# Optimization experiments

Measured on AMD Instinct MI355X. Metric: run time of the kernel, lower is better.

## Reference

```python
import jax, jax.numpy as jnp
import numpy as np

N = 50000      # nodes
E = 1600000    # edges (avg degree 32)
F_IN = 3       # PROTEINS num_node_features
H = 64         # dim_h
G = 512        # num graphs in batch
C = 2          # PROTEINS num_classes
BN_EPS = 1e-5


def setup_inputs() -> dict:
    key = jax.random.key(0)
    ks = iter(jax.random.split(key, 64))

    def rn(shape, s=0.1):
        return (jax.random.normal(next(ks), shape) * s).astype(jnp.float32)

    inp = {"x": rn((N, F_IN), 1.0)}
    for li, din in ((1, F_IN), (2, H), (3, H)):
        p = f"conv{li}_"
        inp[p + "w1"] = rn((din, H))
        inp[p + "b1"] = rn((H,))
        inp[p + "bn_g"] = jnp.ones((H,), jnp.float32)
        inp[p + "bn_b"] = jnp.zeros((H,), jnp.float32)
        inp[p + "bn_m"] = rn((H,))
        inp[p + "bn_v"] = jax.random.uniform(next(ks), (H,), jnp.float32, 0.5, 1.5)
        inp[p + "w2"] = rn((H, H))
        inp[p + "b2"] = rn((H,))
    inp["lin1_w"] = rn((3 * H, 3 * H))
    inp["lin1_b"] = rn((3 * H,))
    inp["lin2_w"] = rn((3 * H, C))
    inp["lin2_b"] = rn((C,))
    inp["edge_index"] = jax.random.randint(next(ks), (2, E), 0, N, jnp.int64)
    inp["batch"] = jnp.sort(jax.random.randint(next(ks), (N,), 0, G, jnp.int64))
    return inp


def gin_conv(x, src, dst, w1, b1, g, bb, m, v, w2, b2):
    # GINConv, eps=0: mlp(x + sum_{j->i} x_j); aggregate messages at target (dst)
    agg = jax.ops.segment_sum(x[src], dst, num_segments=N)  # [N, d]
    h = x + agg
    h = h @ w1 + b1
    h = (h - m) * jax.lax.rsqrt(v + BN_EPS) * g + bb  # BatchNorm1d (eval)
    h = jax.nn.relu(h)
    h = jax.nn.relu(h @ w2 + b2)
    return h


def reference(x,
              conv1_w1, conv1_b1, conv1_bn_g, conv1_bn_b, conv1_bn_m, conv1_bn_v, conv1_w2, conv1_b2,
              conv2_w1, conv2_b1, conv2_bn_g, conv2_bn_b, conv2_bn_m, conv2_bn_v, conv2_w2, conv2_b2,
              conv3_w1, conv3_b1, conv3_bn_g, conv3_bn_b, conv3_bn_m, conv3_bn_v, conv3_w2, conv3_b2,
              lin1_w, lin1_b, lin2_w, lin2_b,
              edge_index, batch):
    src, dst = edge_index[0], edge_index[1]
    h1 = gin_conv(x,  src, dst, conv1_w1, conv1_b1, conv1_bn_g, conv1_bn_b, conv1_bn_m, conv1_bn_v, conv1_w2, conv1_b2)
    h2 = gin_conv(h1, src, dst, conv2_w1, conv2_b1, conv2_bn_g, conv2_bn_b, conv2_bn_m, conv2_bn_v, conv2_w2, conv2_b2)
    h3 = gin_conv(h2, src, dst, conv3_w1, conv3_b1, conv3_bn_g, conv3_bn_b, conv3_bn_m, conv3_bn_v, conv3_w2, conv3_b2)
    # global_add_pool per graph
    p1 = jax.ops.segment_sum(h1, batch, num_segments=G)
    p2 = jax.ops.segment_sum(h2, batch, num_segments=G)
    p3 = jax.ops.segment_sum(h3, batch, num_segments=G)
    h = jnp.concatenate((p1, p2, p3), axis=1)          # [G, 3H]
    h = jax.nn.relu(h @ lin1_w + lin1_b)
    # dropout p=0.5 is identity in eval mode
    h = h @ lin2_w + lin2_b                            # [G, C]
    return (h, jax.nn.log_softmax(h, axis=1))
```

## Files before the change

kernel.cpp:

```cpp
#include <hip/hip_runtime.h>
#include <hip/hip_bf16.h>
#include <math.h>

#define N_NODES 50000
#define N_EDGES 1600000
#define H 64
#define G_GRAPHS 512
#define C_CLS 2
#define BN_EPS 1e-5f
#define NBUCK 196
#define BUCKCAP 16384
#define E4 (N_EDGES / 4)
#define SCHUNKS ((E4 + 511) / 512)
#define XCHUNKS ((N_NODES + 255) / 256)
#define IOP 72
#define ZROW N_NODES
#define HSTRIDE ((N_NODES + 1) * H)

typedef __attribute__((ext_vector_type(8))) short short8;
typedef __attribute__((ext_vector_type(4))) float floatx4;

__device__ __forceinline__ float bflo(unsigned int u) { return __uint_as_float(u << 16); }
__device__ __forceinline__ float bfhi(unsigned int u) { return __uint_as_float(u & 0xffff0000u); }
__device__ __forceinline__ unsigned int bf16_rne(float f) {
    unsigned int u = __float_as_uint(f);
    u += 0x7fffu + ((u >> 16) & 1u);
    return u >> 16;
}

#define RED3(A) { A += __shfl_xor(A, 8); A += __shfl_xor(A, 16); A += __shfl_xor(A, 32); }
#define RED6(A) { A += __shfl_xor(A, 1); A += __shfl_xor(A, 2); A += __shfl_xor(A, 4); \
                  A += __shfl_xor(A, 8); A += __shfl_xor(A, 16); A += __shfl_xor(A, 32); }

__global__ __launch_bounds__(256) void prepscatter_kernel(
    const int* __restrict__ src, const int* __restrict__ dst,
    int* __restrict__ gcnt, int* __restrict__ gpacked,
    const float* __restrict__ w2_0, const float* __restrict__ w1_1,
    const float* __restrict__ w2_1, const float* __restrict__ w1_2,
    const float* __restrict__ w2_2, unsigned short* __restrict__ wt,
    const float* __restrict__ x, uint2* __restrict__ xb,
    __hip_bfloat16* __restrict__ h1, __hip_bfloat16* __restrict__ h2) {
    int b = blockIdx.x, t = threadIdx.x;
    if (b < SCHUNKS) {
        __shared__ int bh[NBUCK];
        if (t < NBUCK) bh[t] = 0;
        __syncthreads();
        int base = b * 512;
        int pkA[4], bkA[4], lrA[4]; bool vA = false;
        int pkB[4], bkB[4], lrB[4]; bool vB = false;
        {
            int i = base + t;
            if (i < E4) {
                vA = true;
                int4 s4 = ((const int4*)src)[i];
                int4 d4 = ((const int4*)dst)[i];
                bkA[0] = d4.x >> 8; pkA[0] = ((d4.x & 255) << 16) | s4.x; lrA[0] = atomicAdd(&bh[bkA[0]], 1);
                bkA[1] = d4.y >> 8; pkA[1] = ((d4.y & 255) << 16) | s4.y; lrA[1] = atomicAdd(&bh[bkA[1]], 1);
                bkA[2] = d4.z >> 8; pkA[2] = ((d4.z & 255) << 16) | s4.z; lrA[2] = atomicAdd(&bh[bkA[2]], 1);
                bkA[3] = d4.w >> 8; pkA[3] = ((d4.w & 255) << 16) | s4.w; lrA[3] = atomicAdd(&bh[bkA[3]], 1);
            }
        }
        {
            int i = base + 256 + t;
            if (i < E4) {
                vB = true;
                int4 s4 = ((const int4*)src)[i];
                int4 d4 = ((const int4*)dst)[i];
                bkB[0] = d4.x >> 8; pkB[0] = ((d4.x & 255) << 16) | s4.x; lrB[0] = atomicAdd(&bh[bkB[0]], 1);
                bkB[1] = d4.y >> 8; pkB[1] = ((d4.y & 255) << 16) | s4.y; lrB[1] = atomicAdd(&bh[bkB[1]], 1);
                bkB[2] = d4.z >> 8; pkB[2] = ((d4.z & 255) << 16) | s4.z; lrB[2] = atomicAdd(&bh[bkB[2]], 1);
                bkB[3] = d4.w >> 8; pkB[3] = ((d4.w & 255) << 16) | s4.w; lrB[3] = atomicAdd(&bh[bkB[3]], 1);
            }
        }
        __syncthreads();
        if (t < NBUCK) {
            int c = bh[t];
            bh[t] = c ? atomicAdd(&gcnt[t], c) : 0;
        }
        __syncthreads();
        if (vA) {
#pragma unroll
            for (int q = 0; q < 4; q++) gpacked[bkA[q] * BUCKCAP + bh[bkA[q]] + lrA[q]] = pkA[q];
        }
        if (vB) {
#pragma unroll
            for (int q = 0; q < 4; q++) gpacked[bkB[q] * BUCKCAP + bh[bkB[q]] + lrB[q]] = pkB[q];
        }
    } else if (b < SCHUNKS + 5) {
        int w_id = b - SCHUNKS;
        const float* w = (w_id == 0) ? w2_0 : (w_id == 1) ? w1_1 : (w_id == 2) ? w2_1
                         : (w_id == 3) ? w1_2 : w2_2;
        unsigned short* o = wt + w_id * (H * H);
        for (int idx = t; idx < H * H; idx += 256) {
            int k = idx >> 6, jc = idx & 63;
            o[jc * H + k] = (unsigned short)bf16_rne(w[idx]);
        }
    } else if (b < SCHUNKS + 5 + XCHUNKS) {
        int node = (b - SCHUNKS - 5) * 256 + t;
        if (node < N_NODES) {
            uint2 p;
            p.x = bf16_rne(x[node * 3 + 0]) | (bf16_rne(x[node * 3 + 1]) << 16);
            p.y = bf16_rne(x[node * 3 + 2]);
            xb[node] = p;
        }
    } else {
        uint4 z = {0u, 0u, 0u, 0u};
        if (t < 8) ((uint4*)((unsigned short*)h1 + (size_t)ZROW * H))[t] = z;
        else if (t < 16) ((uint4*)((unsigned short*)h2 + (size_t)ZROW * H))[t - 8] = z;
        else if (t == 16) { uint2 zz; zz.x = 0u; zz.y = 0u; xb[ZROW] = zz; }
    }
}

__global__ __launch_bounds__(256) void bcsr_kernel(const int* __restrict__ gpacked,
                                                   const int* __restrict__ gcnt,
                                                   int* __restrict__ row_start,
                                                   int* __restrict__ edge_src) {
    __shared__ int cnt[256];
    __shared__ int pref[256];
    int b = blockIdx.x;
    int t = threadIdx.x;

    int v = (t < NBUCK) ? gcnt[t] : 0;
    pref[t] = v;
    __syncthreads();
    for (int off = 1; off < 256; off <<= 1) {
        int u = 0;
        if (t >= off) u = pref[t - off];
        __syncthreads();
        if (t >= off) pref[t] += u;
        __syncthreads();
    }
    int bs = (b > 0) ? pref[b - 1] : 0;
    int cnt_b = gcnt[b];
    if (b == 0 && t == 0) row_start[N_NODES] = N_EDGES;
    __syncthreads();

    const int* gp = gpacked + (size_t)b * BUCKCAP;
    cnt[t] = 0;
    __syncthreads();
    for (int i = t; i < cnt_b; i += 256) atomicAdd(&cnt[gp[i] >> 16], 1);
    __syncthreads();
    int c = cnt[t];
    pref[t] = c;
    __syncthreads();
    for (int off = 1; off < 256; off <<= 1) {
        int u = 0;
        if (t >= off) u = pref[t - off];
        __syncthreads();
        if (t >= off) pref[t] += u;
        __syncthreads();
    }
    int excl = pref[t] - c;
    int node = b * 256 + t;
    if (node < N_NODES) row_start[node] = bs + excl;
    cnt[t] = excl;
    __syncthreads();
    for (int i = t; i < cnt_b; i += 256) {
        int p = gp[i];
        int pos = atomicAdd(&cnt[p >> 16], 1);
        edge_src[bs + pos] = p & 0xffff;
    }
}

__global__ __launch_bounds__(512, 4) void gin1_fused16_kernel(
    const float* __restrict__ x, const uint2* __restrict__ xb,
    const int* __restrict__ row_start, const int* __restrict__ edge_src,
    const float* __restrict__ w1, const float* __restrict__ b1,
    const float* __restrict__ bn_g, const float* __restrict__ bn_b,
    const float* __restrict__ bn_m, const float* __restrict__ bn_v,
    const unsigned short* __restrict__ w2t, const float* __restrict__ b2,
    __hip_bfloat16* __restrict__ hout, const int* __restrict__ batch,
    float* __restrict__ pool) {
    __shared__ unsigned short s_mid[16 * IOP];
    __shared__ unsigned short s_xs[16 * IOP];
    __shared__ int s_bat[16];

    int tid = threadIdx.x;
    int wave = tid >> 6, j = tid & 63;
    int quad = j >> 4, l15 = j & 15;
    int nodebase = blockIdx.x * 16;
    if (tid < 16) s_bat[tid] = batch[nodebase + tid];

    float wj0 = w1[j], wj1 = w1[H + j], wj2 = w1[2 * H + j];
    float sc = rsqrtf(bn_v[j] + BN_EPS) * bn_g[j];
    float sh = bn_b[j] - bn_m[j] * sc;
    float bj = b1[j];

    int n0 = nodebase + wave * 2;
    int rsA = row_start[n0];
    int rsB = row_start[n0 + 1];
    int reB = row_start[n0 + 2];
    int cntA = rsB - rsA, cntB = reB - rsB;
    int cmax = max(cntA, cntB);

    float a0 = 0.f, a1 = 0.f, a2 = 0.f;
    float c0 = 0.f, c1 = 0.f, c2 = 0.f;
    for (int base = 0; base < cmax; base += 64) {
        int iA = base + j;
        int svA = (iA < cntA) ? edge_src[rsA + iA] : ZROW;
        int svB = (iA < cntB) ? edge_src[rsB + iA] : ZROW;
        uint2 pA = xb[svA];
        uint2 pB = xb[svB];
        a0 += bflo(pA.x); a1 += bfhi(pA.x); a2 += bflo(pA.y);
        c0 += bflo(pB.x); c1 += bfhi(pB.x); c2 += bflo(pB.y);
    }
    RED6(a0) RED6(c0) RED6(a1) RED6(c1) RED6(a2) RED6(c2)
    {
        float in0 = a0 + x[n0 * 3 + 0];
        float in1 = a1 + x[n0 * 3 + 1];
        float in2 = a2 + x[n0 * 3 + 2];
        float m = bj + in0 * wj0 + in1 * wj1 + in2 * wj2;
        m = fmaxf(m * sc + sh, 0.f);
        s_mid[(wave * 2) * IOP + j] = (unsigned short)bf16_rne(m);
    }
    {
        int n1 = n0 + 1;
        float in0 = c0 + x[n1 * 3 + 0];
        float in1 = c1 + x[n1 * 3 + 1];
        float in2 = c2 + x[n1 * 3 + 2];
        float m = bj + in0 * wj0 + in1 * wj1 + in2 * wj2;
        m = fmaxf(m * sc + sh, 0.f);
        s_mid[(wave * 2 + 1) * IOP + j] = (unsigned short)bf16_rne(m);
    }
    __syncthreads();

    if (wave < 4) {
        int jj = wave * 16 + l15;
        float bb2 = b2[jj];
        short8 m0 = *(const short8*)&s_mid[l15 * IOP + quad * 8];
        short8 m1 = *(const short8*)&s_mid[l15 * IOP + quad * 8 + 32];
        short8 b0 = *(const short8*)&w2t[jj * H + quad * 8];
        short8 bv = *(const short8*)&w2t[jj * H + quad * 8 + 32];
        floatx4 c = {0.f, 0.f, 0.f, 0.f};
        c = __builtin_amdgcn_mfma_f32_16x16x32_bf16(m0, b0, c, 0, 0, 0);
        c = __builtin_amdgcn_mfma_f32_16x16x32_bf16(m1, bv, c, 0, 0, 0);
        float vv[4];
#pragma unroll
        for (int r = 0; r < 4; r++) {
            vv[r] = fmaxf(c[r] + bb2, 0.f);
            s_xs[(quad * 4 + r) * IOP + jj] = (unsigned short)bf16_rne(vv[r]);
        }
        int bq0 = s_bat[quad * 4], bq3 = s_bat[quad * 4 + 3];
        if (bq0 == bq3) {
            atomicAdd(&pool[bq0 * 192 + jj], (vv[0] + vv[1]) + (vv[2] + vv[3]));
        } else {
            atomicAdd(&pool[s_bat[quad * 4 + 0] * 192 + jj], vv[0]);
            atomicAdd(&pool[s_bat[quad * 4 + 1] * 192 + jj], vv[1]);
            atomicAdd(&pool[s_bat[quad * 4 + 2] * 192 + jj], vv[2]);
            atomicAdd(&pool[s_bat[quad * 4 + 3] * 192 + jj], vv[3]);
        }
    }
    __syncthreads();

    if (wave < 2) {
        int r = wave * 8 + (j >> 3);
        short8 v = *(const short8*)&s_xs[r * IOP + (j & 7) * 8];
        *(short8*)((unsigned short*)hout + (size_t)(nodebase + r) * H + (j & 7) * 8) = v;
    }
}

#define ACCA(R) { \
    a0 += bflo(R.x); a1 += bfhi(R.x); a2 += bflo(R.y); a3 += bfhi(R.y); \
    a4 += bflo(R.z); a5 += bfhi(R.z); a6 += bflo(R.w); a7 += bfhi(R.w); }
#define ACCB(R) { \
    c0 += bflo(R.x); c1 += bfhi(R.x); c2 += bflo(R.y); c3 += bfhi(R.y); \
    c4 += bflo(R.z); c5 += bfhi(R.z); c6 += bflo(R.w); c7 += bfhi(R.w); }
#define GLOAD(R, sv, kk) { int s_ = __shfl(sv, (kk) + o); \
    R = *(const uint4*)(hb + (size_t)s_ * 128 + jo * 16); }

__global__ __launch_bounds__(512, 4) void gin_fused16_kernel(
    const __hip_bfloat16* __restrict__ hin, const int* __restrict__ row_start,
    const int* __restrict__ edge_src,
    const unsigned short* __restrict__ w1t, const float* __restrict__ b1,
    const float* __restrict__ bn_g, const float* __restrict__ bn_b,
    const float* __restrict__ bn_m, const float* __restrict__ bn_v,
    const unsigned short* __restrict__ w2t, const float* __restrict__ b2,
    __hip_bfloat16* __restrict__ hout, const int* __restrict__ batch,
    float* __restrict__ pool) {
    __shared__ unsigned short s_xs[16 * IOP];
    __shared__ unsigned short s_mid[16 * IOP];
    __shared__ int s_bat[16];

    int tid = threadIdx.x;
    int wave = tid >> 6, j = tid & 63;
    int o = j >> 3, jo = j & 7;
    int quad = j >> 4, l15 = j & 15;
    int nodebase = blockIdx.x * 16;
    if (tid < 16) s_bat[tid] = batch[nodebase + tid];

    const char* hb = (const char*)hin;

    int n0 = nodebase + wave * 2;
    int rsA = row_start[n0];
    int rsB = row_start[n0 + 1];
    int reB = row_start[n0 + 2];
    int cntA = rsB - rsA, cntB = reB - rsB;
    int cmax = max(cntA, cntB);

    float a0 = 0.f, a1 = 0.f, a2 = 0.f, a3 = 0.f, a4 = 0.f, a5 = 0.f, a6 = 0.f, a7 = 0.f;
    float c0 = 0.f, c1 = 0.f, c2 = 0.f, c3 = 0.f, c4 = 0.f, c5 = 0.f, c6 = 0.f, c7 = 0.f;

    for (int base = 0; base < cmax; base += 64) {
        int iA = base + j;
        int svA = (iA < cntA) ? edge_src[rsA + iA] : ZROW;
        int svB = (iA < cntB) ? edge_src[rsB + iA] : ZROW;
        bool dA0 = base < cntA,      eA0 = base + 8 < cntA;
        bool dA1 = base + 16 < cntA, eA1 = base + 24 < cntA;
        bool dA2 = base + 32 < cntA, eA2 = base + 40 < cntA;
        bool dA3 = base + 48 < cntA, eA3 = base + 56 < cntA;
        bool dB0 = base < cntB,      eB0 = base + 8 < cntB;
        bool dB1 = base + 16 < cntB, eB1 = base + 24 < cntB;
        bool dB2 = base + 32 < cntB, eB2 = base + 40 < cntB;
        bool dB3 = base + 48 < cntB, eB3 = base + 56 < cntB;
        uint4 PA0, PA1, PB0, PB1, QA0, QA1, QB0, QB1;
        if (dA0) GLOAD(PA0, svA, 0)
        if (eA0) GLOAD(PA1, svA, 8)
        if (dB0) GLOAD(PB0, svB, 0)
        if (eB0) GLOAD(PB1, svB, 8)
        if (dA1) GLOAD(QA0, svA, 16)
        if (eA1) GLOAD(QA1, svA, 24)
        if (dB1) GLOAD(QB0, svB, 16)
        if (eB1) GLOAD(QB1, svB, 24)
        if (dA0) ACCA(PA0)
        if (eA0) ACCA(PA1)
        if (dB0) ACCB(PB0)
        if (eB0) ACCB(PB1)
        if (dA2) GLOAD(PA0, svA, 32)
        if (eA2) GLOAD(PA1, svA, 40)
        if (dB2) GLOAD(PB0, svB, 32)
        if (eB2) GLOAD(PB1, svB, 40)
        if (dA1) ACCA(QA0)
        if (eA1) ACCA(QA1)
        if (dB1) ACCB(QB0)
        if (eB1) ACCB(QB1)
        if (dA3) GLOAD(QA0, svA, 48)
        if (eA3) GLOAD(QA1, svA, 56)
        if (dB3) GLOAD(QB0, svB, 48)
        if (eB3) GLOAD(QB1, svB, 56)
        if (dA2) ACCA(PA0)
        if (eA2) ACCA(PA1)
        if (dB2) ACCB(PB0)
        if (eB2) ACCB(PB1)
        if (dA3) ACCA(QA0)
        if (eA3) ACCA(QA1)
        if (dB3) ACCB(QB0)
        if (eB3) ACCB(QB1)
    }
    RED3(a0) RED3(c0) RED3(a1) RED3(c1) RED3(a2) RED3(c2) RED3(a3) RED3(c3)
    RED3(a4) RED3(c4) RED3(a5) RED3(c5) RED3(a6) RED3(c6) RED3(a7) RED3(c7)

    if (o < 2) {
        int nl = wave * 2 + o;
        float r0 = (o == 0) ? a0 : c0, r1 = (o == 0) ? a1 : c1;
        float r2 = (o == 0) ? a2 : c2, r3 = (o == 0) ? a3 : c3;
        float r4 = (o == 0) ? a4 : c4, r5 = (o == 0) ? a5 : c5;
        float r6 = (o == 0) ? a6 : c6, r7 = (o == 0) ? a7 : c7;
        uint4 raw = *(const uint4*)(hb + (size_t)(nodebase + nl) * 128 + jo * 16);
        r0 += bflo(raw.x); r1 += bfhi(raw.x);
        r2 += bflo(raw.y); r3 += bfhi(raw.y);
        r4 += bflo(raw.z); r5 += bfhi(raw.z);
        r6 += bflo(raw.w); r7 += bfhi(raw.w);
        uint4 ov;
        ov.x = bf16_rne(r0) | (bf16_rne(r1) << 16);
        ov.y = bf16_rne(r2) | (bf16_rne(r3) << 16);
        ov.z = bf16_rne(r4) | (bf16_rne(r5) << 16);
        ov.w = bf16_rne(r6) | (bf16_rne(r7) << 16);
        *(uint4*)&s_xs[nl * IOP + jo * 8] = ov;
    }
    __syncthreads();

    int jj = (wave & 3) * 16 + l15;
    float scv, shv, bb1, bb2;
    if (wave < 4) {
        scv = rsqrtf(bn_v[jj] + BN_EPS) * bn_g[jj];
        shv = bn_b[jj] - bn_m[jj] * scv;
        bb1 = b1[jj];
        bb2 = b2[jj];
        short8 A0 = *(const short8*)&s_xs[l15 * IOP + quad * 8];
        short8 A1 = *(const short8*)&s_xs[l15 * IOP + quad * 8 + 32];
        short8 w10 = *(const short8*)&w1t[jj * H + quad * 8];
        short8 w11 = *(const short8*)&w1t[jj * H + quad * 8 + 32];
        floatx4 c = {0.f, 0.f, 0.f, 0.f};
        c = __builtin_amdgcn_mfma_f32_16x16x32_bf16(A0, w10, c, 0, 0, 0);
        c = __builtin_amdgcn_mfma_f32_16x16x32_bf16(A1, w11, c, 0, 0, 0);
#pragma unroll
        for (int r = 0; r < 4; r++) {
            float v = (c[r] + bb1) * scv + shv;
            v = fmaxf(v, 0.f);
            s_mid[(quad * 4 + r) * IOP + jj] = (unsigned short)bf16_rne(v);
        }
    }
    __syncthreads();

    if (wave < 4) {
        short8 M0 = *(const short8*)&s_mid[l15 * IOP + quad * 8];
        short8 M1 = *(const short8*)&s_mid[l15 * IOP + quad * 8 + 32];
        short8 w20 = *(const short8*)&w2t[jj * H + quad * 8];
        short8 w21 = *(const short8*)&w2t[jj * H + quad * 8 + 32];
        floatx4 c2 = {0.f, 0.f, 0.f, 0.f};
        c2 = __builtin_amdgcn_mfma_f32_16x16x32_bf16(M0, w20, c2, 0, 0, 0);
        c2 = __builtin_amdgcn_mfma_f32_16x16x32_bf16(M1, w21, c2, 0, 0, 0);
        float vv[4];
#pragma unroll
        for (int r = 0; r < 4; r++) {
            vv[r] = fmaxf(c2[r] + bb2, 0.f);
            s_xs[(quad * 4 + r) * IOP + jj] = (unsigned short)bf16_rne(vv[r]);
        }
        int bq0 = s_bat[quad * 4], bq3 = s_bat[quad * 4 + 3];
        if (bq0 == bq3) {
            atomicAdd(&pool[bq0 * 192 + jj], (vv[0] + vv[1]) + (vv[2] + vv[3]));
        } else {
            atomicAdd(&pool[s_bat[quad * 4 + 0] * 192 + jj], vv[0]);
            atomicAdd(&pool[s_bat[quad * 4 + 1] * 192 + jj], vv[1]);
            atomicAdd(&pool[s_bat[quad * 4 + 2] * 192 + jj], vv[2]);
            atomicAdd(&pool[s_bat[quad * 4 + 3] * 192 + jj], vv[3]);
        }
    }
    __syncthreads();

    if (wave < 2) {
        int r = wave * 8 + (j >> 3);
        short8 v = *(const short8*)&s_xs[r * IOP + (j & 7) * 8];
        *(short8*)((unsigned short*)hout + (size_t)(nodebase + r) * H + (j & 7) * 8) = v;
    }
}

__global__ __launch_bounds__(192) void head_kernel(
    const float* __restrict__ pool,
    const float* __restrict__ lin1_w, const float* __restrict__ lin1_b,
    const float* __restrict__ lin2_w, const float* __restrict__ lin2_b,
    float* __restrict__ out) {
    __shared__ float s_row[3 * H];
    __shared__ float s_mid[3 * H];
    __shared__ float s_z[C_CLS];

    int g = blockIdx.x;
    int j = threadIdx.x;
    s_row[j] = pool[g * 192 + j];
    __syncthreads();

    float acc = lin1_b[j];
    for (int k = 0; k < 3 * H; k++) acc += s_row[k] * lin1_w[k * (3 * H) + j];
    s_mid[j] = fmaxf(acc, 0.f);
    __syncthreads();

    if (j < C_CLS) {
        float z = lin2_b[j];
        for (int k = 0; k < 3 * H; k++) z += s_mid[k] * lin2_w[k * C_CLS + j];
        s_z[j] = z;
    }
    __syncthreads();
    if (j < C_CLS) {
        float z0 = s_z[0], z1 = s_z[1];
        float mx = fmaxf(z0, z1);
        float lse = mx + logf(expf(z0 - mx) + expf(z1 - mx));
        out[g * C_CLS + j] = s_z[j];
        out[G_GRAPHS * C_CLS + g * C_CLS + j] = s_z[j] - lse;
    }
}

extern "C" void kernel_launch(void* const* d_in, const int* in_sizes, int n_in,
                              void* d_out, int out_size, void* d_ws, size_t ws_size,
                              hipStream_t stream) {
    const float* x = (const float*)d_in[0];
    const float* cw1[3], *cb1[3], *cg[3], *cbb[3], *cm[3], *cv[3], *cw2[3], *cb2[3];
    for (int l = 0; l < 3; l++) {
        int b = 1 + 8 * l;
        cw1[l] = (const float*)d_in[b + 0];
        cb1[l] = (const float*)d_in[b + 1];
        cg[l]  = (const float*)d_in[b + 2];
        cbb[l] = (const float*)d_in[b + 3];
        cm[l]  = (const float*)d_in[b + 4];
        cv[l]  = (const float*)d_in[b + 5];
        cw2[l] = (const float*)d_in[b + 6];
        cb2[l] = (const float*)d_in[b + 7];
    }
    const float* lin1_w = (const float*)d_in[25];
    const float* lin1_b = (const float*)d_in[26];
    const float* lin2_w = (const float*)d_in[27];
    const float* lin2_b = (const float*)d_in[28];
    const int* edge_index = (const int*)d_in[29];
    const int* batch = (const int*)d_in[30];
    const int* src = edge_index;
    const int* dst = edge_index + N_EDGES;
    float* out = (float*)d_out;

    int* edge_src = (int*)d_ws;
    int* gpacked = edge_src + N_EDGES;
    int* gcnt = gpacked + (size_t)NBUCK * BUCKCAP;
    float* pool = (float*)(gcnt + NBUCK);
    int* row_start = (int*)(pool + G_GRAPHS * 3 * H);
    uintptr_t hp = (uintptr_t)(row_start + N_NODES + 2);
    hp = (hp + 127) & ~(uintptr_t)127;
    unsigned short* wt = (unsigned short*)hp;
    uint2* xb = (uint2*)(wt + 5 * H * H);
    __hip_bfloat16* h1 = (__hip_bfloat16*)(xb + N_NODES + 1);
    __hip_bfloat16* h2 = h1 + (size_t)HSTRIDE;
    __hip_bfloat16* h3 = h2 + (size_t)HSTRIDE;

    const unsigned short* w2t_0 = wt + 0 * H * H;
    const unsigned short* w1t_1 = wt + 1 * H * H;
    const unsigned short* w2t_1 = wt + 2 * H * H;
    const unsigned short* w1t_2 = wt + 3 * H * H;
    const unsigned short* w2t_2 = wt + 4 * H * H;

    hipMemsetAsync(gcnt, 0, NBUCK * sizeof(int) + (size_t)G_GRAPHS * 3 * H * sizeof(float),
                   stream);
    prepscatter_kernel<<<SCHUNKS + 5 + XCHUNKS + 1, 256, 0, stream>>>(
        src, dst, gcnt, gpacked, cw2[0], cw1[1], cw2[1], cw1[2], cw2[2], wt, x, xb, h1, h2);
    bcsr_kernel<<<NBUCK, 256, 0, stream>>>(gpacked, gcnt, row_start, edge_src);

    const int fgrid = N_NODES / 16;

    gin1_fused16_kernel<<<fgrid, 512, 0, stream>>>(x, xb, row_start, edge_src,
        cw1[0], cb1[0], cg[0], cbb[0], cm[0], cv[0], w2t_0, cb2[0], h1, batch, pool);
    gin_fused16_kernel<<<fgrid, 512, 0, stream>>>(h1, row_start, edge_src,
        w1t_1, cb1[1], cg[1], cbb[1], cm[1], cv[1], w2t_1, cb2[1], h2, batch, pool + 64);
    gin_fused16_kernel<<<fgrid, 512, 0, stream>>>(h2, row_start, edge_src,
        w1t_2, cb1[2], cg[2], cbb[2], cm[2], cv[2], w2t_2, cb2[2], h3, batch, pool + 128);
    head_kernel<<<G_GRAPHS, 3 * H, 0, stream>>>(pool,
        lin1_w, lin1_b, lin2_w, lin2_b, out);
}
```

Baseline: 329.6 us.

## Run the node MLP in one wave and use branch-free neighbour gathers

The per-block MLP stage (both GEMMs, pooling atomics and the output store) now runs on a single wave that loops over four column tiles, instead of being spread over four waves with block-wide barriers in between. This removes two __syncthreads and the shared-memory round trip between waves. The neighbour-gather loop drops its per-load predicates and always issues all 16 loads, relying on padding indices that point at a zero row. The min-blocks-per-CU hint is removed from launch_bounds. In exchange, the MLP work is serialised on one wave, and low-degree nodes issue extra redundant loads.

```diff
diff --git a/kernel.cpp b/kernel.cpp
--- a/kernel.cpp
+++ b/kernel.cpp
@@ -162,7 +162,7 @@
     }
 }
 
-__global__ __launch_bounds__(512, 4) void gin1_fused16_kernel(
+__global__ __launch_bounds__(512) void gin1_fused16_kernel(
     const float* __restrict__ x, const uint2* __restrict__ xb,
     const int* __restrict__ row_start, const int* __restrict__ edge_src,
     const float* __restrict__ w1, const float* __restrict__ b1,
@@ -172,12 +172,10 @@
     __hip_bfloat16* __restrict__ hout, const int* __restrict__ batch,
     float* __restrict__ pool) {
     __shared__ unsigned short s_mid[16 * IOP];
-    __shared__ unsigned short s_xs[16 * IOP];
     __shared__ int s_bat[16];
 
     int tid = threadIdx.x;
     int wave = tid >> 6, j = tid & 63;
-    int quad = j >> 4, l15 = j & 15;
     int nodebase = blockIdx.x * 16;
     if (tid < 16) s_bat[tid] = batch[nodebase + tid];
 
@@ -224,38 +222,46 @@
     }
     __syncthreads();
 
-    if (wave < 4) {
-        int jj = wave * 16 + l15;
-        float bb2 = b2[jj];
+    if (wave == 0) {
+        int quad = j >> 4, l15 = j & 15;
+        float bb2[4];
+#pragma unroll
+        for (int jt = 0; jt < 4; jt++) bb2[jt] = b2[jt * 16 + l15];
+
         short8 m0 = *(const short8*)&s_mid[l15 * IOP + quad * 8];
         short8 m1 = *(const short8*)&s_mid[l15 * IOP + quad * 8 + 32];
-        short8 b0 = *(const short8*)&w2t[jj * H + quad * 8];
-        short8 bv = *(const short8*)&w2t[jj * H + quad * 8 + 32];
-        floatx4 c = {0.f, 0.f, 0.f, 0.f};
-        c = __builtin_amdgcn_mfma_f32_16x16x32_bf16(m0, b0, c, 0, 0, 0);
-        c = __builtin_amdgcn_mfma_f32_16x16x32_bf16(m1, bv, c, 0, 0, 0);
-        float vv[4];
-#pragma unroll
-        for (int r = 0; r < 4; r++) {
-            vv[r] = fmaxf(c[r] + bb2, 0.f);
-            s_xs[(quad * 4 + r) * IOP + jj] = (unsigned short)bf16_rne(vv[r]);
-        }
         int bq0 = s_bat[quad * 4], bq3 = s_bat[quad * 4 + 3];
-        if (bq0 == bq3) {
-            atomicAdd(&pool[bq0 * 192 + jj], (vv[0] + vv[1]) + (vv[2] + vv[3]));
-        } else {
-            atomicAdd(&pool[s_bat[quad * 4 + 0] * 192 + jj], vv[0]);
-            atomicAdd(&pool[s_bat[quad * 4 + 1] * 192 + jj], vv[1]);
-            atomicAdd(&pool[s_bat[quad * 4 + 2] * 192 + jj], vv[2]);
-            atomicAdd(&pool[s_bat[quad * 4 + 3] * 192 + jj], vv[3]);
-        }
-    }
-    __syncthreads();
-
-    if (wave < 2) {
-        int r = wave * 8 + (j >> 3);
-        short8 v = *(const short8*)&s_xs[r * IOP + (j & 7) * 8];
-        *(short8*)((unsigned short*)hout + (size_t)(nodebase + r) * H + (j & 7) * 8) = v;
+#pragma unroll
+        for (int jt = 0; jt < 4; jt++) {
+            short8 b0 = *(const short8*)&w2t[(jt * 16 + l15) * H + quad * 8];
+            short8 bv = *(const short8*)&w2t[(jt * 16 + l15) * H + quad * 8 + 32];
+            floatx4 c = {0.f, 0.f, 0.f, 0.f};
+            c = __builtin_amdgcn_mfma_f32_16x16x32_bf16(m0, b0, c, 0, 0, 0);
+            c = __builtin_amdgcn_mfma_f32_16x16x32_bf16(m1, bv, c, 0, 0, 0);
+            float vv[4];
+#pragma unroll
+            for (int r = 0; r < 4; r++) {
+                float v = fmaxf(c[r] + bb2[jt], 0.f);
+                vv[r] = v;
+                s_mid[(quad * 4 + r) * IOP + jt * 16 + l15] = (unsigned short)bf16_rne(v);
+            }
+            int jj = jt * 16 + l15;
+            if (bq0 == bq3) {
+                atomicAdd(&pool[bq0 * 192 + jj], (vv[0] + vv[1]) + (vv[2] + vv[3]));
+            } else {
+                atomicAdd(&pool[s_bat[quad * 4 + 0] * 192 + jj], vv[0]);
+                atomicAdd(&pool[s_bat[quad * 4 + 1] * 192 + jj], vv[1]);
+                atomicAdd(&pool[s_bat[quad * 4 + 2] * 192 + jj], vv[2]);
+                atomicAdd(&pool[s_bat[quad * 4 + 3] * 192 + jj], vv[3]);
+            }
+        }
+        unsigned short* ho = (unsigned short*)hout;
+#pragma unroll
+        for (int cc = 0; cc < 2; cc++) {
+            int r = cc * 8 + (j >> 3);
+            short8 v = *(const short8*)&s_mid[r * IOP + (j & 7) * 8];
+            *(short8*)(ho + (size_t)(nodebase + r) * H + (j & 7) * 8) = v;
+        }
     }
 }
 
@@ -268,7 +274,7 @@
 #define GLOAD(R, sv, kk) { int s_ = __shfl(sv, (kk) + o); \
     R = *(const uint4*)(hb + (size_t)s_ * 128 + jo * 16); }
 
-__global__ __launch_bounds__(512, 4) void gin_fused16_kernel(
+__global__ __launch_bounds__(512) void gin_fused16_kernel(
     const __hip_bfloat16* __restrict__ hin, const int* __restrict__ row_start,
     const int* __restrict__ edge_src,
     const unsigned short* __restrict__ w1t, const float* __restrict__ b1,
@@ -284,7 +290,6 @@
     int tid = threadIdx.x;
     int wave = tid >> 6, j = tid & 63;
     int o = j >> 3, jo = j & 7;
-    int quad = j >> 4, l15 = j & 15;
     int nodebase = blockIdx.x * 16;
     if (tid < 16) s_bat[tid] = batch[nodebase + tid];
 
@@ -304,47 +309,24 @@
         int iA = base + j;
         int svA = (iA < cntA) ? edge_src[rsA + iA] : ZROW;
         int svB = (iA < cntB) ? edge_src[rsB + iA] : ZROW;
-        bool dA0 = base < cntA,      eA0 = base + 8 < cntA;
-        bool dA1 = base + 16 < cntA, eA1 = base + 24 < cntA;
-        bool dA2 = base + 32 < cntA, eA2 = base + 40 < cntA;
-        bool dA3 = base + 48 < cntA, eA3 = base + 56 < cntA;
-        bool dB0 = base < cntB,      eB0 = base + 8 < cntB;
-        bool dB1 = base + 16 < cntB, eB1 = base + 24 < cntB;
-        bool dB2 = base + 32 < cntB, eB2 = base + 40 < cntB;
-        bool dB3 = base + 48 < cntB, eB3 = base + 56 < cntB;
-        uint4 PA0, PA1, PB0, PB1, QA0, QA1, QB0, QB1;
-        if (dA0) GLOAD(PA0, svA, 0)
-        if (eA0) GLOAD(PA1, svA, 8)
-        if (dB0) GLOAD(PB0, svB, 0)
-        if (eB0) GLOAD(PB1, svB, 8)
-        if (dA1) GLOAD(QA0, svA, 16)
-        if (eA1) GLOAD(QA1, svA, 24)
-        if (dB1) GLOAD(QB0, svB, 16)
-        if (eB1) GLOAD(QB1, svB, 24)
-        if (dA0) ACCA(PA0)
-        if (eA0) ACCA(PA1)
-        if (dB0) ACCB(PB0)
-        if (eB0) ACCB(PB1)
-        if (dA2) GLOAD(PA0, svA, 32)
-        if (eA2) GLOAD(PA1, svA, 40)
-        if (dB2) GLOAD(PB0, svB, 32)
-        if (eB2) GLOAD(PB1, svB, 40)
-        if (dA1) ACCA(QA0)
-        if (eA1) ACCA(QA1)
-        if (dB1) ACCB(QB0)
-        if (eB1) ACCB(QB1)
-        if (dA3) GLOAD(QA0, svA, 48)
-        if (eA3) GLOAD(QA1, svA, 56)
-        if (dB3) GLOAD(QB0, svB, 48)
-        if (eB3) GLOAD(QB1, svB, 56)
-        if (dA2) ACCA(PA0)
-        if (eA2) ACCA(PA1)
-        if (dB2) ACCB(PB0)
-        if (eB2) ACCB(PB1)
-        if (dA3) ACCA(QA0)
-        if (eA3) ACCA(QA1)
-        if (dB3) ACCB(QB0)
-        if (eB3) ACCB(QB1)
+        uint4 RA0, RA1, RA2, RA3, RA4, RA5, RA6, RA7;
+        uint4 RB0, RB1, RB2, RB3, RB4, RB5, RB6, RB7;
+        GLOAD(RA0, svA, 0)  GLOAD(RB0, svB, 0)
+        GLOAD(RA1, svA, 8)  GLOAD(RB1, svB, 8)
+        GLOAD(RA2, svA, 16) GLOAD(RB2, svB, 16)
+        GLOAD(RA3, svA, 24) GLOAD(RB3, svB, 24)
+        GLOAD(RA4, svA, 32) GLOAD(RB4, svB, 32)
+        GLOAD(RA5, svA, 40) GLOAD(RB5, svB, 40)
+        GLOAD(RA6, svA, 48) GLOAD(RB6, svB, 48)
+        GLOAD(RA7, svA, 56) GLOAD(RB7, svB, 56)
+        ACCA(RA0) ACCB(RB0)
+        ACCA(RA1) ACCB(RB1)
+        ACCA(RA2) ACCB(RB2)
+        ACCA(RA3) ACCB(RB3)
+        ACCA(RA4) ACCB(RB4)
+        ACCA(RA5) ACCB(RB5)
+        ACCA(RA6) ACCB(RB6)
+        ACCA(RA7) ACCB(RB7)
     }
     RED3(a0) RED3(c0) RED3(a1) RED3(c1) RED3(a2) RED3(c2) RED3(a3) RED3(c3)
     RED3(a4) RED3(c4) RED3(a5) RED3(c5) RED3(a6) RED3(c6) RED3(a7) RED3(c7)
@@ -369,59 +351,68 @@
     }
     __syncthreads();
 
-    int jj = (wave & 3) * 16 + l15;
-    float scv, shv, bb1, bb2;
-    if (wave < 4) {
-        scv = rsqrtf(bn_v[jj] + BN_EPS) * bn_g[jj];
-        shv = bn_b[jj] - bn_m[jj] * scv;
-        bb1 = b1[jj];
-        bb2 = b2[jj];
-        short8 A0 = *(const short8*)&s_xs[l15 * IOP + quad * 8];
-        short8 A1 = *(const short8*)&s_xs[l15 * IOP + quad * 8 + 32];
-        short8 w10 = *(const short8*)&w1t[jj * H + quad * 8];
-        short8 w11 = *(const short8*)&w1t[jj * H + quad * 8 + 32];
-        floatx4 c = {0.f, 0.f, 0.f, 0.f};
-        c = __builtin_amdgcn_mfma_f32_16x16x32_bf16(A0, w10, c, 0, 0, 0);
-        c = __builtin_amdgcn_mfma_f32_16x16x32_bf16(A1, w11, c, 0, 0, 0);
-#pragma unroll
-        for (int r = 0; r < 4; r++) {
-            float v = (c[r] + bb1) * scv + shv;
-            v = fmaxf(v, 0.f);
-            s_mid[(quad * 4 + r) * IOP + jj] = (unsigned short)bf16_rne(v);
-        }
-    }
-    __syncthreads();
-
-    if (wave < 4) {
-        short8 M0 = *(const short8*)&s_mid[l15 * IOP + quad * 8];
-        short8 M1 = *(const short8*)&s_mid[l15 * IOP + quad * 8 + 32];
-        short8 w20 = *(const short8*)&w2t[jj * H + quad * 8];
-        short8 w21 = *(const short8*)&w2t[jj * H + quad * 8 + 32];
-        floatx4 c2 = {0.f, 0.f, 0.f, 0.f};
-        c2 = __builtin_amdgcn_mfma_f32_16x16x32_bf16(M0, w20, c2, 0, 0, 0);
-        c2 = __builtin_amdgcn_mfma_f32_16x16x32_bf16(M1, w21, c2, 0, 0, 0);
-        float vv[4];
-#pragma unroll
-        for (int r = 0; r < 4; r++) {
-            vv[r] = fmaxf(c2[r] + bb2, 0.f);
-            s_xs[(quad * 4 + r) * IOP + jj] = (unsigned short)bf16_rne(vv[r]);
-        }
+    if (wave == 0) {
+        int quad = j >> 4, l15 = j & 15;
+        float scl[4], sht[4], bb1[4], bb2[4];
+#pragma unroll
+        for (int jt = 0; jt < 4; jt++) {
+            int jj = jt * 16 + l15;
+            float sc = rsqrtf(bn_v[jj] + BN_EPS) * bn_g[jj];
+            scl[jt] = sc;
+            sht[jt] = bn_b[jj] - bn_m[jj] * sc;
+            bb1[jt] = b1[jj];
+            bb2[jt] = b2[jj];
+        }
+        short8 a0v = *(const short8*)&s_xs[l15 * IOP + quad * 8];
+        short8 a1v = *(const short8*)&s_xs[l15 * IOP + quad * 8 + 32];
+#pragma unroll
+        for (int jt = 0; jt < 4; jt++) {
+            short8 b0 = *(const short8*)&w1t[(jt * 16 + l15) * H + quad * 8];
+            short8 bv = *(const short8*)&w1t[(jt * 16 + l15) * H + quad * 8 + 32];
+            floatx4 c = {0.f, 0.f, 0.f, 0.f};
+            c = __builtin_amdgcn_mfma_f32_16x16x32_bf16(a0v, b0, c, 0, 0, 0);
+            c = __builtin_amdgcn_mfma_f32_16x16x32_bf16(a1v, bv, c, 0, 0, 0);
+#pragma unroll
+            for (int r = 0; r < 4; r++) {
+                float v = (c[r] + bb1[jt]) * scl[jt] + sht[jt];
+                v = fmaxf(v, 0.f);
+                s_mid[(quad * 4 + r) * IOP + jt * 16 + l15] = (unsigned short)bf16_rne(v);
+            }
+        }
+        short8 m0 = *(const short8*)&s_mid[l15 * IOP + quad * 8];
+        short8 m1 = *(const short8*)&s_mid[l15 * IOP + quad * 8 + 32];
         int bq0 = s_bat[quad * 4], bq3 = s_bat[quad * 4 + 3];
-        if (bq0 == bq3) {
-            atomicAdd(&pool[bq0 * 192 + jj], (vv[0] + vv[1]) + (vv[2] + vv[3]));
-        } else {
-            atomicAdd(&pool[s_bat[quad * 4 + 0] * 192 + jj], vv[0]);
-            atomicAdd(&pool[s_bat[quad * 4 + 1] * 192 + jj], vv[1]);
-            atomicAdd(&pool[s_bat[quad * 4 + 2] * 192 + jj], vv[2]);
-            atomicAdd(&pool[s_bat[quad * 4 + 3] * 192 + jj], vv[3]);
-        }
-    }
-    __syncthreads();
-
-    if (wave < 2) {
-        int r = wave * 8 + (j >> 3);
-        short8 v = *(const short8*)&s_xs[r * IOP + (j & 7) * 8];
-        *(short8*)((unsigned short*)hout + (size_t)(nodebase + r) * H + (j & 7) * 8) = v;
+#pragma unroll
+        for (int jt = 0; jt < 4; jt++) {
+            short8 b0 = *(const short8*)&w2t[(jt * 16 + l15) * H + quad * 8];
+            short8 bv = *(const short8*)&w2t[(jt * 16 + l15) * H + quad * 8 + 32];
+            floatx4 c = {0.f, 0.f, 0.f, 0.f};
+            c = __builtin_amdgcn_mfma_f32_16x16x32_bf16(m0, b0, c, 0, 0, 0);
+            c = __builtin_amdgcn_mfma_f32_16x16x32_bf16(m1, bv, c, 0, 0, 0);
+            float vv[4];
+#pragma unroll
+            for (int r = 0; r < 4; r++) {
+                float v = fmaxf(c[r] + bb2[jt], 0.f);
+                vv[r] = v;
+                s_xs[(quad * 4 + r) * IOP + jt * 16 + l15] = (unsigned short)bf16_rne(v);
+            }
+            int jj = jt * 16 + l15;
+            if (bq0 == bq3) {
+                atomicAdd(&pool[bq0 * 192 + jj], (vv[0] + vv[1]) + (vv[2] + vv[3]));
+            } else {
+                atomicAdd(&pool[s_bat[quad * 4 + 0] * 192 + jj], vv[0]);
+                atomicAdd(&pool[s_bat[quad * 4 + 1] * 192 + jj], vv[1]);
+                atomicAdd(&pool[s_bat[quad * 4 + 2] * 192 + jj], vv[2]);
+                atomicAdd(&pool[s_bat[quad * 4 + 3] * 192 + jj], vv[3]);
+            }
+        }
+        unsigned short* ho = (unsigned short*)hout;
+#pragma unroll
+        for (int cc = 0; cc < 2; cc++) {
+            int r = cc * 8 + (j >> 3);
+            short8 v = *(const short8*)&s_xs[r * IOP + (j & 7) * 8];
+            *(short8*)(ho + (size_t)(nodebase + r) * H + (j & 7) * 8) = v;
+        }
     }
 }
 
```

Result: no change. 323.5 us (-1.9%).
